# Performance work log

Measured on AMD Instinct MI355X. Metric: run time of the kernel, lower is better.

## Reference

```python
import jax, jax.numpy as jnp
import numpy as np

DIM = 512
NUM_HEADS = 16
HEAD_DIM = DIM // NUM_HEADS
WINDOW = 256
MEM = 16  # memory tokens
NEG_INF = -1e30


def setup_inputs() -> dict:
    key = jax.random.key(0)
    ks = jax.random.split(key, 12)
    B, S, D = 2, 2048, DIM
    inp = {
        "query": jax.random.normal(ks[0], (B, S, D), jnp.float32),
        "key": jax.random.normal(ks[1], (B, S, D), jnp.float32),
        "value": jax.random.normal(ks[2], (B, S, D), jnp.float32),
        # persistent memory tokens, init N(0, 0.02)
        "mem": 0.02 * jax.random.normal(ks[3], (1, MEM, D), jnp.float32),
        # linear layers (stored as [in, out]; x @ W + b)
        "Wq": jax.random.normal(ks[4], (D, D), jnp.float32) / np.sqrt(D),
        "bq": jnp.zeros((D,), jnp.float32),
        "Wk": jax.random.normal(ks[5], (D, D), jnp.float32) / np.sqrt(D),
        "bk": jnp.zeros((D,), jnp.float32),
        "Wv": jax.random.normal(ks[6], (D, D), jnp.float32) / np.sqrt(D),
        "bv": jnp.zeros((D,), jnp.float32),
        "Wo": jax.random.normal(ks[7], (D, D), jnp.float32) / np.sqrt(D),
        "bo": jnp.zeros((D,), jnp.float32),
    }
    return inp


def _sliding_mask(seq_len):
    # additive mask for [MEM + seq_len] tokens: memory rows/cols fully visible,
    # content-content limited to |i-j| <= window//2
    T = seq_len + MEM
    w2 = WINDOW // 2
    i = jnp.arange(T)[:, None]
    j = jnp.arange(T)[None, :]
    allowed = (i < MEM) | (j < MEM) | (jnp.abs(i - j) <= w2)
    return jnp.where(allowed, 0.0, NEG_INF).astype(jnp.float32)


def reference(query, key, value, mem, Wq, bq, Wk, bk, Wv, bv, Wo, bo):
    B, S, D = query.shape
    scale = HEAD_DIM ** -0.5
    m = jnp.broadcast_to(mem, (B, MEM, D))
    qm = jnp.concatenate([m, query], axis=1)  # [B, T, D]
    km = jnp.concatenate([m, key], axis=1)
    vm = jnp.concatenate([m, value], axis=1)
    T = S + MEM

    def heads(x, W, b):
        y = x @ W + b
        return y.reshape(B, T, NUM_HEADS, HEAD_DIM).transpose(0, 2, 1, 3)  # [B,H,T,hd]

    q = heads(qm, Wq, bq)
    k = heads(km, Wk, bk)
    v = heads(vm, Wv, bv)

    mask = _sliding_mask(S)[None, None]  # [1,1,T,T]
    scores = jnp.einsum("bhqd,bhkd->bhqk", q, k) * scale + mask
    weights = jax.nn.softmax(scores, axis=-1)
    ctx = jnp.einsum("bhqk,bhkd->bhqd", weights, v)
    ctx = ctx.transpose(0, 2, 1, 3).reshape(B, T, D)
    ctx = ctx[:, MEM:]  # drop memory tokens
    return ctx @ Wo + bo
```

## Files before the change

### kernel.cpp

```cpp
#include <hip/hip_runtime.h>
#include <hip/hip_bf16.h>
#include <hip/hip_fp16.h>

#define DIM 512
#define NUM_HEADS 16
#define HEAD_DIM 32
#define WHALF 128
#define MEMN 16
#define SEQ 2048
#define BATCH 2
#define T_TOT (SEQ + MEMN)
#define MROWS (BATCH * T_TOT)
#define OROWS (BATCH * SEQ)
#define QT 128
#define MAXU 416
#define KSTR 40
#define VSTR 424

typedef _Float16 f16x8 __attribute__((ext_vector_type(8)));
typedef __fp16   f16raw2 __attribute__((ext_vector_type(2)));
typedef float    f32x4 __attribute__((ext_vector_type(4)));

#define QSCALE 0.17677669529663687f

__global__ __launch_bounds__(256) void prep_cvt(
    const float* __restrict__ q, const float* __restrict__ k,
    const float* __restrict__ v, const float* __restrict__ memp,
    const float* __restrict__ Wq, const float* __restrict__ Wk,
    const float* __restrict__ Wv, const float* __restrict__ Wo,
    ushort* __restrict__ Xq, ushort* __restrict__ Xk, ushort* __restrict__ Xv,
    ushort* __restrict__ Wtq, ushort* __restrict__ Wtk,
    ushort* __restrict__ Wtv, ushort* __restrict__ Wto)
{
    const int z = blockIdx.z;
    if (z < 3) {
        const float* X = z == 0 ? q : (z == 1 ? k : v);
        ushort*     Xc = z == 0 ? Xq : (z == 1 ? Xk : Xv);
        const int gid  = blockIdx.x * 256 + threadIdx.x;
        const int base = gid * 8;
        if (base >= MROWS * DIM) return;
        const int row = base >> 9;
        const int c   = base & 511;
        const int b   = row / T_TOT;
        const int t   = row - b * T_TOT;
        const float* src = (t < MEMN)
            ? (memp + (size_t)t * DIM + c)
            : (X + ((size_t)b * SEQ + (t - MEMN)) * DIM + c);
        const float4 a0 = *(const float4*)src;
        const float4 a1 = *(const float4*)(src + 4);
        union { _Float16 hh[8]; uint4 u4; } o;
        o.hh[0] = (_Float16)a0.x; o.hh[1] = (_Float16)a0.y;
        o.hh[2] = (_Float16)a0.z; o.hh[3] = (_Float16)a0.w;
        o.hh[4] = (_Float16)a1.x; o.hh[5] = (_Float16)a1.y;
        o.hh[6] = (_Float16)a1.z; o.hh[7] = (_Float16)a1.w;
        *(uint4*)(Xc + (size_t)row * DIM + c) = o.u4;
        return;
    }
    if (blockIdx.x >= 64) return;
    const int w = z - 3;
    const float* W  = w == 0 ? Wq  : (w == 1 ? Wk  : (w == 2 ? Wv  : Wo));
    ushort*     Wt  = w == 0 ? Wtq : (w == 1 ? Wtk : (w == 2 ? Wtv : Wto));
    const float ws  = (w == 0) ? QSCALE : 1.0f;

    __shared__ float sT[64][65];
    const int n0 = (blockIdx.x & 7) * 64;
    const int k0 = (blockIdx.x >> 3) * 64;

    for (int e = threadIdx.x; e < 1024; e += 256) {
        const int r  = e >> 4;
        const int c4 = e & 15;
        const float4 f = *(const float4*)(W + (size_t)(k0 + r) * DIM + n0 + c4 * 4);
        sT[r][c4 * 4 + 0] = f.x;
        sT[r][c4 * 4 + 1] = f.y;
        sT[r][c4 * 4 + 2] = f.z;
        sT[r][c4 * 4 + 3] = f.w;
    }
    __syncthreads();
    for (int u = threadIdx.x; u < 512; u += 256) {
        const int n  = u >> 3;
        const int kg = u & 7;
        union { ushort us[8]; uint4 u4; } o;
        #pragma unroll
        for (int j = 0; j < 8; ++j) {
            _Float16 h = (_Float16)(sT[kg * 8 + j][n] * ws);
            o.us[j] = *(ushort*)&h;
        }
        *(uint4*)(Wt + (size_t)(n0 + n) * DIM + k0 + kg * 8) = o.u4;
    }
}

__device__ __forceinline__ void gemm_body128(
    const ushort* __restrict__ A, const ushort* __restrict__ Bt,
    const float* __restrict__ bias, float bscale, ushort* __restrict__ C, int M)
{
    __shared__ _Float16 sA[128][72];
    __shared__ _Float16 sB[128][72];

    const int tid  = threadIdx.x;
    const int row0 = blockIdx.x * 128;
    const int col0 = blockIdx.y * 128;
    const int wave = tid >> 6, lane = tid & 63;
    const int wr = wave >> 1, wc = wave & 1;
    const int fr = lane & 15, fq = lane >> 4;

    f32x4 acc[4][4];
    #pragma unroll
    for (int n = 0; n < 4; ++n) {
        const float bb = bias[col0 + wc * 64 + n * 16 + fr] * bscale;
        #pragma unroll
        for (int m = 0; m < 4; ++m) acc[m][n] = (f32x4){bb, bb, bb, bb};
    }

    for (int k0 = 0; k0 < 512; k0 += 64) {
        __syncthreads();
        #pragma unroll
        for (int it = 0; it < 8; ++it) {
            const int u  = tid + it * 256;
            const int r  = (u >> 3) & 127;
            const int cc = u & 7;
            if (u < 1024) {
                int gr = row0 + r; if (gr >= M) gr = M - 1;
                *(uint4*)&sA[r][cc * 8] =
                    *(const uint4*)(A + (size_t)gr * 512 + k0 + cc * 8);
            } else {
                *(uint4*)&sB[r][cc * 8] =
                    *(const uint4*)(Bt + (size_t)(col0 + r) * 512 + k0 + cc * 8);
            }
        }
        __syncthreads();
        #pragma unroll
        for (int kk = 0; kk < 2; ++kk) {
            f16x8 a[4], b[4];
            #pragma unroll
            for (int m = 0; m < 4; ++m)
                a[m] = *(const f16x8*)&sA[wr * 64 + m * 16 + fr][kk * 32 + fq * 8];
            #pragma unroll
            for (int n = 0; n < 4; ++n)
                b[n] = *(const f16x8*)&sB[wc * 64 + n * 16 + fr][kk * 32 + fq * 8];
            #pragma unroll
            for (int m = 0; m < 4; ++m)
                #pragma unroll
                for (int n = 0; n < 4; ++n)
                    acc[m][n] = __builtin_amdgcn_mfma_f32_16x16x32_f16(
                        a[m], b[n], acc[m][n], 0, 0, 0);
        }
    }

    #pragma unroll
    for (int m = 0; m < 4; ++m)
        #pragma unroll
        for (int n = 0; n < 4; ++n)
            #pragma unroll
            for (int j = 0; j < 4; ++j) {
                const int row = row0 + wr * 64 + m * 16 + fq * 4 + j;
                const int col = col0 + wc * 64 + n * 16 + fr;
                if (row < M) {
                    _Float16 h = (_Float16)acc[m][n][j];
                    C[(size_t)row * 512 + col] = *(ushort*)&h;
                }
            }
}

__global__ __launch_bounds__(256) void gemm_qkv(
    const ushort* __restrict__ Xq, const ushort* __restrict__ Xk,
    const ushort* __restrict__ Xv,
    const ushort* __restrict__ Wtq, const ushort* __restrict__ Wtk,
    const ushort* __restrict__ Wtv,
    const float* __restrict__ bq, const float* __restrict__ bk,
    const float* __restrict__ bv,
    ushort* __restrict__ Qc, ushort* __restrict__ Kc, ushort* __restrict__ Vc)
{
    const int w = blockIdx.z;
    const ushort* A  = w == 0 ? Xq  : (w == 1 ? Xk  : Xv);
    const ushort* Bt = w == 0 ? Wtq : (w == 1 ? Wtk : Wtv);
    const float*  bi = w == 0 ? bq  : (w == 1 ? bk  : bv);
    ushort*       Cc = w == 0 ? Qc  : (w == 1 ? Kc  : Vc);
    gemm_body128(A, Bt, bi, (w == 0) ? QSCALE : 1.0f, Cc, MROWS);
}

__global__ __launch_bounds__(256) void gemm_out64(
    const ushort* __restrict__ A, const ushort* __restrict__ Bt,
    const float* __restrict__ bias, float* __restrict__ C)
{
    __shared__ _Float16 sA[64][72];
    __shared__ _Float16 sB[128][72];

    const int tid  = threadIdx.x;
    const int row0 = blockIdx.x * 64;
    const int col0 = blockIdx.y * 128;
    const int wave = tid >> 6, lane = tid & 63;
    const int wr = wave >> 1, wc = wave & 1;
    const int fr = lane & 15, fq = lane >> 4;

    f32x4 acc[2][4];
    #pragma unroll
    for (int n = 0; n < 4; ++n) {
        const float bb = bias[col0 + wc * 64 + n * 16 + fr];
        #pragma unroll
        for (int m = 0; m < 2; ++m) acc[m][n] = (f32x4){bb, bb, bb, bb};
    }

    for (int k0 = 0; k0 < 512; k0 += 64) {
        __syncthreads();
        #pragma unroll
        for (int it = 0; it < 6; ++it) {
            const int u  = tid + it * 256;
            const int cc = u & 7;
            if (u < 512) {
                const int r = u >> 3;
                *(uint4*)&sA[r][cc * 8] =
                    *(const uint4*)(A + (size_t)(row0 + r) * 512 + k0 + cc * 8);
            } else {
                const int r = (u - 512) >> 3;
                *(uint4*)&sB[r][cc * 8] =
                    *(const uint4*)(Bt + (size_t)(col0 + r) * 512 + k0 + cc * 8);
            }
        }
        __syncthreads();
        #pragma unroll
        for (int kk = 0; kk < 2; ++kk) {
            f16x8 a[2], b[4];
            #pragma unroll
            for (int m = 0; m < 2; ++m)
                a[m] = *(const f16x8*)&sA[wr * 32 + m * 16 + fr][kk * 32 + fq * 8];
            #pragma unroll
            for (int n = 0; n < 4; ++n)
                b[n] = *(const f16x8*)&sB[wc * 64 + n * 16 + fr][kk * 32 + fq * 8];
            #pragma unroll
            for (int m = 0; m < 2; ++m)
                #pragma unroll
                for (int n = 0; n < 4; ++n)
                    acc[m][n] = __builtin_amdgcn_mfma_f32_16x16x32_f16(
                        a[m], b[n], acc[m][n], 0, 0, 0);
        }
    }

    #pragma unroll
    for (int m = 0; m < 2; ++m)
        #pragma unroll
        for (int n = 0; n < 4; ++n)
            #pragma unroll
            for (int j = 0; j < 4; ++j) {
                const int row = row0 + wr * 32 + m * 16 + fq * 4 + j;
                const int col = col0 + wc * 64 + n * 16 + fr;
                C[(size_t)row * 512 + col] = acc[m][n][j];
            }
}

__global__ __launch_bounds__(512, 4) void attn_mfma(
    const ushort* __restrict__ Q, const ushort* __restrict__ K,
    const ushort* __restrict__ V, ushort* __restrict__ ctx)
{
    const int tid  = threadIdx.x;
    const int tile = blockIdx.x, h = blockIdx.y, b = blockIdx.z;
    const int wave = tid >> 6, lane = tid & 63;
    const int fr = lane & 15, fq = lane >> 4;
    const int fq8 = fq * 8, fq4 = fq * 4;

    const int i0  = MEMN + tile * QT;
    const int klo = max(MEMN, i0 - WHALF);
    const int khi = min(T_TOT - 1, i0 + QT - 1 + WHALF);
    const int total  = MEMN + khi - klo + 1;
    const int ustage = (total + 31) & ~31;

    __shared__ ushort sK[MAXU][KSTR];
    __shared__ ushort sVt[HEAD_DIM][VSTR];

    const size_t hbase = (size_t)b * T_TOT * DIM + (size_t)h * HEAD_DIM;

    for (int idx = tid; idx < ustage * 4; idx += 512) {
        const int u = idx >> 2, c = idx & 3;
        const int cc = (c + u) & 3;
        uint4 val = {0, 0, 0, 0};
        if (u < total) {
            const int g = (u < MEMN) ? u : klo + u - MEMN;
            val = *(const uint4*)(K + hbase + (size_t)g * DIM + cc * 8);
        }
        *(uint4*)&sK[u][cc * 8] = val;
    }
    for (int idx = tid; idx < (ustage / 2) * 4; idx += 512) {
        const int pr = idx >> 2;
        const int u2 = pr * 2, c = idx & 3;
        union { uint4 q4; ushort us[8]; } r0, r1;
        r0.q4 = (uint4){0, 0, 0, 0};
        r1.q4 = (uint4){0, 0, 0, 0};
        if (u2 < total) {
            const int g0 = (u2 < MEMN) ? u2 : klo + u2 - MEMN;
            r0.q4 = *(const uint4*)(V + hbase + (size_t)g0 * DIM + c * 8);
        }
        if (u2 + 1 < total) {
            const int g1 = (u2 + 1 < MEMN) ? u2 + 1 : klo + u2 + 1 - MEMN;
            r1.q4 = *(const uint4*)(V + hbase + (size_t)g1 * DIM + c * 8);
        }
        const int g  = u2 & 31, gb = u2 & ~31;
        const int w  = (g < 16) ? ((g >> 2) * 4 + ((g >> 1) & 1))
                                : (((g - 16) >> 2) * 4 + 2 + (((g - 16) >> 1) & 1));
        const int col = gb + w * 2;
        #pragma unroll
        for (int ii = 0; ii < 8; ++ii) {
            const int i = (ii + pr + 2 * c) & 7;
            const uint wv = (uint)r0.us[i] | ((uint)r1.us[i] << 16);
            *(uint*)&sVt[c * 8 + i][col] = wv;
        }
    }

    const int iq = i0 + wave * 16 + fr;
    const f16x8 qf = *(const f16x8*)(Q + (size_t)(b * T_TOT + iq) * DIM
                                     + h * HEAD_DIM + fq8);

    const int ulo  = max(iq - WHALF - klo, 0) + MEMN;
    const int uhi  = min(iq + WHALF, khi) - klo + MEMN;
    const int span = uhi - ulo;
    const int iw0  = i0 + wave * 16;
    const int ulo_minw = max(iw0 - WHALF - klo, 0) + MEMN;
    const int ulo_maxw = max(iw0 + 15 - WHALF - klo, 0) + MEMN;
    const int uhi_minw = min(iw0 + WHALF, khi) - klo + MEMN;
    const int uhi_maxw = min(iw0 + 15 + WHALF, khi) - klo + MEMN;
    const int glo = max(1, ulo_minw >> 5);
    const int ghi = uhi_maxw >> 5;

    __syncthreads();

    const float NEGINF = -__builtin_huge_valf();
    float mns = 0.0f;
    float l   = 0.f;
    f32x4 oc0 = {0, 0, 0, 0}, oc1 = {0, 0, 0, 0};

    {
        const f16x8 kfA = *(const f16x8*)&sK[fr][fq8];
        const f16x8 kfB = *(const f16x8*)&sK[16 + fr][fq8];
        f32x4 sA = {0, 0, 0, 0}, sB = {0, 0, 0, 0};
        sA = __builtin_amdgcn_mfma_f32_16x16x32_f16(kfA, qf, sA, 0, 0, 0);
        sB = __builtin_amdgcn_mfma_f32_16x16x32_f16(kfB, qf, sB, 0, 0, 0);
        if (!(16 >= ulo_maxw && 31 <= uhi_minw)) {
            #pragma unroll
            for (int j = 0; j < 4; ++j) {
                const uint uu = (uint)(16 + fq4 + j - ulo);
                sB[j] = (uu <= (uint)span) ? sB[j] : NEGINF;
            }
        }
        float mx = fmaxf(fmaxf(fmaxf(sA[0], sA[1]), fmaxf(sA[2], sA[3])),
                         fmaxf(fmaxf(sB[0], sB[1]), fmaxf(sB[2], sB[3])));
        mx = fmaxf(mx, __shfl_xor(mx, 16));
        mx = fmaxf(mx, __shfl_xor(mx, 32));
        if (!__all(mx <= mns)) {
            const float mn2   = fmaxf(mns, mx);
            const float alpha = __expf(mns - mn2);
            l *= alpha;
            #pragma unroll
            for (int j = 0; j < 4; ++j) { oc0[j] *= alpha; oc1[j] *= alpha; }
            mns = mn2;
        }
        const float p0 = __expf(sA[0] - mns), p1 = __expf(sA[1] - mns);
        const float p2 = __expf(sA[2] - mns), p3 = __expf(sA[3] - mns);
        const float p4 = __expf(sB[0] - mns), p5 = __expf(sB[1] - mns);
        const float p6 = __expf(sB[2] - mns), p7 = __expf(sB[3] - mns);
        l += ((p0 + p1) + (p2 + p3)) + ((p4 + p5) + (p6 + p7));
        union { f16raw2 h2; uint u; } c0, c1, c2, c3;
        c0.h2 = __builtin_amdgcn_cvt_pkrtz(p0, p1);
        c1.h2 = __builtin_amdgcn_cvt_pkrtz(p2, p3);
        c2.h2 = __builtin_amdgcn_cvt_pkrtz(p4, p5);
        c3.h2 = __builtin_amdgcn_cvt_pkrtz(p6, p7);
        union { uint u[4]; f16x8 h; } P;
        P.u[0] = c0.u; P.u[1] = c1.u; P.u[2] = c2.u; P.u[3] = c3.u;
        const f16x8 va0 = *(const f16x8*)&sVt[fr][fq8];
        const f16x8 va1 = *(const f16x8*)&sVt[fr + 16][fq8];
        oc0 = __builtin_amdgcn_mfma_f32_16x16x32_f16(va0, P.h, oc0, 0, 0, 0);
        oc1 = __builtin_amdgcn_mfma_f32_16x16x32_f16(va1, P.h, oc1, 0, 0, 0);
    }

    int g = glo;
    for (; g + 1 <= ghi; g += 2) {
        const int ua = g * 32, ub2 = ua + 32;
        const f16x8 kf0 = *(const f16x8*)&sK[ua + fr][fq8];
        const f16x8 kf1 = *(const f16x8*)&sK[ua + 16 + fr][fq8];
        const f16x8 kf2 = *(const f16x8*)&sK[ub2 + fr][fq8];
        const f16x8 kf3 = *(const f16x8*)&sK[ub2 + 16 + fr][fq8];
        f32x4 s0 = {0,0,0,0}, s1 = {0,0,0,0}, s2 = {0,0,0,0}, s3 = {0,0,0,0};
        s0 = __builtin_amdgcn_mfma_f32_16x16x32_f16(kf0, qf, s0, 0, 0, 0);
        s1 = __builtin_amdgcn_mfma_f32_16x16x32_f16(kf1, qf, s1, 0, 0, 0);
        s2 = __builtin_amdgcn_mfma_f32_16x16x32_f16(kf2, qf, s2, 0, 0, 0);
        s3 = __builtin_amdgcn_mfma_f32_16x16x32_f16(kf3, qf, s3, 0, 0, 0);
        #pragma unroll
        for (int cch = 0; cch < 4; ++cch) {
            const int base = ua + cch * 16;
            f32x4& sc = cch == 0 ? s0 : (cch == 1 ? s1 : (cch == 2 ? s2 : s3));
            if (!(base >= ulo_maxw && base + 15 <= uhi_minw)) {
                #pragma unroll
                for (int j = 0; j < 4; ++j) {
                    const uint uu = (uint)(base + fq4 + j - ulo);
                    sc[j] = (uu <= (uint)span) ? sc[j] : NEGINF;
                }
            }
        }
        float mxA = fmaxf(fmaxf(fmaxf(s0[0], s0[1]), fmaxf(s0[2], s0[3])),
                          fmaxf(fmaxf(s1[0], s1[1]), fmaxf(s1[2], s1[3])));
        float mxB = fmaxf(fmaxf(fmaxf(s2[0], s2[1]), fmaxf(s2[2], s2[3])),
                          fmaxf(fmaxf(s3[0], s3[1]), fmaxf(s3[2], s3[3])));
        float mx = fmaxf(mxA, mxB);
        mx = fmaxf(mx, __shfl_xor(mx, 16));
        mx = fmaxf(mx, __shfl_xor(mx, 32));
        if (!__all(mx <= mns)) {
            const float mn2   = fmaxf(mns, mx);
            const float alpha = __expf(mns - mn2);
            l *= alpha;
            #pragma unroll
            for (int j = 0; j < 4; ++j) { oc0[j] *= alpha; oc1[j] *= alpha; }
            mns = mn2;
        }
        const float a0 = __expf(s0[0] - mns), a1 = __expf(s0[1] - mns);
        const float a2 = __expf(s0[2] - mns), a3 = __expf(s0[3] - mns);
        const float a4 = __expf(s1[0] - mns), a5 = __expf(s1[1] - mns);
        const float a6 = __expf(s1[2] - mns), a7 = __expf(s1[3] - mns);
        const float b0 = __expf(s2[0] - mns), b1 = __expf(s2[1] - mns);
        const float b2 = __expf(s2[2] - mns), b3 = __expf(s2[3] - mns);
        const float b4 = __expf(s3[0] - mns), b5 = __expf(s3[1] - mns);
        const float b6 = __expf(s3[2] - mns), b7 = __expf(s3[3] - mns);
        l += (((a0 + a1) + (a2 + a3)) + ((a4 + a5) + (a6 + a7)))
           + (((b0 + b1) + (b2 + b3)) + ((b4 + b5) + (b6 + b7)));
        union { f16raw2 h2; uint u; } d0, d1, d2, d3, e0, e1, e2, e3;
        d0.h2 = __builtin_amdgcn_cvt_pkrtz(a0, a1);
        d1.h2 = __builtin_amdgcn_cvt_pkrtz(a2, a3);
        d2.h2 = __builtin_amdgcn_cvt_pkrtz(a4, a5);
        d3.h2 = __builtin_amdgcn_cvt_pkrtz(a6, a7);
        e0.h2 = __builtin_amdgcn_cvt_pkrtz(b0, b1);
        e1.h2 = __builtin_amdgcn_cvt_pkrtz(b2, b3);
        e2.h2 = __builtin_amdgcn_cvt_pkrtz(b4, b5);
        e3.h2 = __builtin_amdgcn_cvt_pkrtz(b6, b7);
        union { uint u[4]; f16x8 h; } P0, P1;
        P0.u[0] = d0.u; P0.u[1] = d1.u; P0.u[2] = d2.u; P0.u[3] = d3.u;
        P1.u[0] = e0.u; P1.u[1] = e1.u; P1.u[2] = e2.u; P1.u[3] = e3.u;
        const f16x8 va0a = *(const f16x8*)&sVt[fr][ua + fq8];
        const f16x8 va1a = *(const f16x8*)&sVt[fr + 16][ua + fq8];
        const f16x8 va0b = *(const f16x8*)&sVt[fr][ub2 + fq8];
        const f16x8 va1b = *(const f16x8*)&sVt[fr + 16][ub2 + fq8];
        oc0 = __builtin_amdgcn_mfma_f32_16x16x32_f16(va0a, P0.h, oc0, 0, 0, 0);
        oc1 = __builtin_amdgcn_mfma_f32_16x16x32_f16(va1a, P0.h, oc1, 0, 0, 0);
        oc0 = __builtin_amdgcn_mfma_f32_16x16x32_f16(va0b, P1.h, oc0, 0, 0, 0);
        oc1 = __builtin_amdgcn_mfma_f32_16x16x32_f16(va1b, P1.h, oc1, 0, 0, 0);
    }
    if (g <= ghi) {
        const int ua = g * 32;
        const f16x8 kf0 = *(const f16x8*)&sK[ua + fr][fq8];
        const f16x8 kf1 = *(const f16x8*)&sK[ua + 16 + fr][fq8];
        f32x4 s0 = {0,0,0,0}, s1 = {0,0,0,0};
        s0 = __builtin_amdgcn_mfma_f32_16x16x32_f16(kf0, qf, s0, 0, 0, 0);
        s1 = __builtin_amdgcn_mfma_f32_16x16x32_f16(kf1, qf, s1, 0, 0, 0);
        #pragma unroll
        for (int cch = 0; cch < 2; ++cch) {
            const int base = ua + cch * 16;
            f32x4& sc = cch == 0 ? s0 : s1;
            if (!(base >= ulo_maxw && base + 15 <= uhi_minw)) {
                #pragma unroll
                for (int j = 0; j < 4; ++j) {
                    const uint uu = (uint)(base + fq4 + j - ulo);
                    sc[j] = (uu <= (uint)span) ? sc[j] : NEGINF;
                }
            }
        }
        float mx = fmaxf(fmaxf(fmaxf(s0[0], s0[1]), fmaxf(s0[2], s0[3])),
                         fmaxf(fmaxf(s1[0], s1[1]), fmaxf(s1[2], s1[3])));
        mx = fmaxf(mx, __shfl_xor(mx, 16));
        mx = fmaxf(mx, __shfl_xor(mx, 32));
        if (!__all(mx <= mns)) {
            const float mn2   = fmaxf(mns, mx);
            const float alpha = __expf(mns - mn2);
            l *= alpha;
            #pragma unroll
            for (int j = 0; j < 4; ++j) { oc0[j] *= alpha; oc1[j] *= alpha; }
            mns = mn2;
        }
        const float p0 = __expf(s0[0] - mns), p1 = __expf(s0[1] - mns);
        const float p2 = __expf(s0[2] - mns), p3 = __expf(s0[3] - mns);
        const float p4 = __expf(s1[0] - mns), p5 = __expf(s1[1] - mns);
        const float p6 = __expf(s1[2] - mns), p7 = __expf(s1[3] - mns);
        l += ((p0 + p1) + (p2 + p3)) + ((p4 + p5) + (p6 + p7));
        union { f16raw2 h2; uint u; } c0, c1, c2, c3;
        c0.h2 = __builtin_amdgcn_cvt_pkrtz(p0, p1);
        c1.h2 = __builtin_amdgcn_cvt_pkrtz(p2, p3);
        c2.h2 = __builtin_amdgcn_cvt_pkrtz(p4, p5);
        c3.h2 = __builtin_amdgcn_cvt_pkrtz(p6, p7);
        union { uint u[4]; f16x8 h; } P;
        P.u[0] = c0.u; P.u[1] = c1.u; P.u[2] = c2.u; P.u[3] = c3.u;
        const f16x8 va0 = *(const f16x8*)&sVt[fr][ua + fq8];
        const f16x8 va1 = *(const f16x8*)&sVt[fr + 16][ua + fq8];
        oc0 = __builtin_amdgcn_mfma_f32_16x16x32_f16(va0, P.h, oc0, 0, 0, 0);
        oc1 = __builtin_amdgcn_mfma_f32_16x16x32_f16(va1, P.h, oc1, 0, 0, 0);
    }

    l += __shfl_xor(l, 16);
    l += __shfl_xor(l, 32);
    const float inv = 1.0f / l;
    union { f16raw2 h2; uint u; } w00, w01, w10, w11;
    w00.h2 = __builtin_amdgcn_cvt_pkrtz(oc0[0] * inv, oc0[1] * inv);
    w01.h2 = __builtin_amdgcn_cvt_pkrtz(oc0[2] * inv, oc0[3] * inv);
    w10.h2 = __builtin_amdgcn_cvt_pkrtz(oc1[0] * inv, oc1[1] * inv);
    w11.h2 = __builtin_amdgcn_cvt_pkrtz(oc1[2] * inv, oc1[3] * inv);
    ushort* cp = ctx + ((size_t)b * SEQ + (iq - MEMN)) * DIM
               + h * HEAD_DIM + fq4;
    *(uint2*)cp        = (uint2){w00.u, w01.u};
    *(uint2*)(cp + 16) = (uint2){w10.u, w11.u};
}

extern "C" void kernel_launch(void* const* d_in, const int* in_sizes, int n_in,
                              void* d_out, int out_size, void* d_ws, size_t ws_size,
                              hipStream_t stream) {
    const float* q    = (const float*)d_in[0];
    const float* k    = (const float*)d_in[1];
    const float* v    = (const float*)d_in[2];
    const float* memp = (const float*)d_in[3];
    const float* Wq   = (const float*)d_in[4];
    const float* bq   = (const float*)d_in[5];
    const float* Wk   = (const float*)d_in[6];
    const float* bk   = (const float*)d_in[7];
    const float* Wv   = (const float*)d_in[8];
    const float* bv   = (const float*)d_in[9];
    const float* Wo   = (const float*)d_in[10];
    const float* bo   = (const float*)d_in[11];
    float* out = (float*)d_out;

    const size_t NX = (size_t)MROWS * DIM;
    const size_t NW = (size_t)DIM * DIM;
    const size_t NC = (size_t)OROWS * DIM;

    ushort* p   = (ushort*)d_ws;
    ushort* Xq  = p;            p += NX;
    ushort* Xk  = p;            p += NX;
    ushort* Xv  = p;            p += NX;
    ushort* Qc  = p;            p += NX;
    ushort* Kc  = p;            p += NX;
    ushort* Vc  = p;            p += NX;
    ushort* Wtq = p;            p += NW;
    ushort* Wtk = p;            p += NW;
    ushort* Wtv = p;            p += NW;
    ushort* Wto = p;            p += NW;
    ushort* Cc  = p;            p += NC;

    dim3 gp((MROWS * DIM / 8 + 255) / 256, 1, 7);
    prep_cvt<<<gp, 256, 0, stream>>>(q, k, v, memp, Wq, Wk, Wv, Wo,
                                     Xq, Xk, Xv, Wtq, Wtk, Wtv, Wto);

    dim3 g1((MROWS + 127) / 128, 4, 3);
    gemm_qkv<<<g1, 256, 0, stream>>>(Xq, Xk, Xv, Wtq, Wtk, Wtv,
                                     bq, bk, bv, Qc, Kc, Vc);

    dim3 g2(SEQ / QT, NUM_HEADS, BATCH);
    attn_mfma<<<g2, 512, 0, stream>>>(Qc, Kc, Vc, Cc);

    dim3 g3(OROWS / 64, 4, 1);
    gemm_out64<<<g3, 256, 0, stream>>>(Cc, Wto, bo, out);
}
```

Before: 80.68 us.

## Store V row-major and read transposed via ds_read_b64_tr_b16; shrink QKV GEMM tiles

The attention kernel now stages V row-major in two 16-column planes and uses the gfx950 LDS transpose-read instruction to build the MFMA A-operand. This replaces the scalar transposing scatter into sVt during staging. The transposed reads are issued early, with an explicit lgkmcnt wait placed before the PV MFMAs. Separately, the QKV GEMM switches to 64-row tiles through a shared templated body that the output GEMM also uses, which doubles the grid for better CU occupancy at the cost of more reloading of B tiles.

```diff
diff --git a/kernel.cpp b/kernel.cpp
--- a/kernel.cpp
+++ b/kernel.cpp
@@ -15,13 +15,20 @@
 #define QT 128
 #define MAXU 416
 #define KSTR 40
-#define VSTR 424
+#define VPLANE (MAXU * 16 * 2)
 
 typedef _Float16 f16x8 __attribute__((ext_vector_type(8)));
 typedef __fp16   f16raw2 __attribute__((ext_vector_type(2)));
 typedef float    f32x4 __attribute__((ext_vector_type(4)));
+typedef uint     u32x2 __attribute__((ext_vector_type(2)));
 
 #define QSCALE 0.17677669529663687f
+
+__device__ __forceinline__ u32x2 tr64(uint addr) {
+    u32x2 r;
+    asm volatile("ds_read_b64_tr_b16 %0, %1" : "=v"(r) : "v"(addr));
+    return r;
+}
 
 __global__ __launch_bounds__(256) void prep_cvt(
     const float* __restrict__ q, const float* __restrict__ k,
@@ -89,40 +96,42 @@
     }
 }
 
-__device__ __forceinline__ void gemm_body128(
+template<bool OUT_HALF>
+__device__ __forceinline__ void gemm_body64(
     const ushort* __restrict__ A, const ushort* __restrict__ Bt,
-    const float* __restrict__ bias, float bscale, ushort* __restrict__ C, int M)
+    const float* __restrict__ bias, float bscale, void* __restrict__ C, int M)
 {
-    __shared__ _Float16 sA[128][72];
+    __shared__ _Float16 sA[64][72];
     __shared__ _Float16 sB[128][72];
 
     const int tid  = threadIdx.x;
-    const int row0 = blockIdx.x * 128;
+    const int row0 = blockIdx.x * 64;
     const int col0 = blockIdx.y * 128;
     const int wave = tid >> 6, lane = tid & 63;
     const int wr = wave >> 1, wc = wave & 1;
     const int fr = lane & 15, fq = lane >> 4;
 
-    f32x4 acc[4][4];
+    f32x4 acc[2][4];
     #pragma unroll
     for (int n = 0; n < 4; ++n) {
         const float bb = bias[col0 + wc * 64 + n * 16 + fr] * bscale;
         #pragma unroll
-        for (int m = 0; m < 4; ++m) acc[m][n] = (f32x4){bb, bb, bb, bb};
+        for (int m = 0; m < 2; ++m) acc[m][n] = (f32x4){bb, bb, bb, bb};
     }
 
     for (int k0 = 0; k0 < 512; k0 += 64) {
         __syncthreads();
         #pragma unroll
-        for (int it = 0; it < 8; ++it) {
+        for (int it = 0; it < 6; ++it) {
             const int u  = tid + it * 256;
-            const int r  = (u >> 3) & 127;
             const int cc = u & 7;
-            if (u < 1024) {
+            if (u < 512) {
+                const int r = u >> 3;
                 int gr = row0 + r; if (gr >= M) gr = M - 1;
                 *(uint4*)&sA[r][cc * 8] =
                     *(const uint4*)(A + (size_t)gr * 512 + k0 + cc * 8);
             } else {
+                const int r = (u - 512) >> 3;
                 *(uint4*)&sB[r][cc * 8] =
                     *(const uint4*)(Bt + (size_t)(col0 + r) * 512 + k0 + cc * 8);
             }
@@ -130,15 +139,15 @@
         __syncthreads();
         #pragma unroll
         for (int kk = 0; kk < 2; ++kk) {
-            f16x8 a[4], b[4];
-            #pragma unroll
-            for (int m = 0; m < 4; ++m)
-                a[m] = *(const f16x8*)&sA[wr * 64 + m * 16 + fr][kk * 32 + fq * 8];
+            f16x8 a[2], b[4];
+            #pragma unroll
+            for (int m = 0; m < 2; ++m)
+                a[m] = *(const f16x8*)&sA[wr * 32 + m * 16 + fr][kk * 32 + fq * 8];
             #pragma unroll
             for (int n = 0; n < 4; ++n)
                 b[n] = *(const f16x8*)&sB[wc * 64 + n * 16 + fr][kk * 32 + fq * 8];
             #pragma unroll
-            for (int m = 0; m < 4; ++m)
+            for (int m = 0; m < 2; ++m)
                 #pragma unroll
                 for (int n = 0; n < 4; ++n)
                     acc[m][n] = __builtin_amdgcn_mfma_f32_16x16x32_f16(
@@ -147,16 +156,20 @@
     }
 
     #pragma unroll
-    for (int m = 0; m < 4; ++m)
+    for (int m = 0; m < 2; ++m)
         #pragma unroll
         for (int n = 0; n < 4; ++n)
             #pragma unroll
             for (int j = 0; j < 4; ++j) {
-                const int row = row0 + wr * 64 + m * 16 + fq * 4 + j;
+                const int row = row0 + wr * 32 + m * 16 + fq * 4 + j;
                 const int col = col0 + wc * 64 + n * 16 + fr;
                 if (row < M) {
-                    _Float16 h = (_Float16)acc[m][n][j];
-                    C[(size_t)row * 512 + col] = *(ushort*)&h;
+                    if (OUT_HALF) {
+                        _Float16 h = (_Float16)acc[m][n][j];
+                        ((ushort*)C)[(size_t)row * 512 + col] = *(ushort*)&h;
+                    } else {
+                        ((float*)C)[(size_t)row * 512 + col] = acc[m][n][j];
+                    }
                 }
             }
 }
@@ -175,76 +188,14 @@
     const ushort* Bt = w == 0 ? Wtq : (w == 1 ? Wtk : Wtv);
     const float*  bi = w == 0 ? bq  : (w == 1 ? bk  : bv);
     ushort*       Cc = w == 0 ? Qc  : (w == 1 ? Kc  : Vc);
-    gemm_body128(A, Bt, bi, (w == 0) ? QSCALE : 1.0f, Cc, MROWS);
+    gemm_body64<true>(A, Bt, bi, (w == 0) ? QSCALE : 1.0f, Cc, MROWS);
 }
 
 __global__ __launch_bounds__(256) void gemm_out64(
     const ushort* __restrict__ A, const ushort* __restrict__ Bt,
     const float* __restrict__ bias, float* __restrict__ C)
 {
-    __shared__ _Float16 sA[64][72];
-    __shared__ _Float16 sB[128][72];
-
-    const int tid  = threadIdx.x;
-    const int row0 = blockIdx.x * 64;
-    const int col0 = blockIdx.y * 128;
-    const int wave = tid >> 6, lane = tid & 63;
-    const int wr = wave >> 1, wc = wave & 1;
-    const int fr = lane & 15, fq = lane >> 4;
-
-    f32x4 acc[2][4];
-    #pragma unroll
-    for (int n = 0; n < 4; ++n) {
-        const float bb = bias[col0 + wc * 64 + n * 16 + fr];
-        #pragma unroll
-        for (int m = 0; m < 2; ++m) acc[m][n] = (f32x4){bb, bb, bb, bb};
-    }
-
-    for (int k0 = 0; k0 < 512; k0 += 64) {
-        __syncthreads();
-        #pragma unroll
-        for (int it = 0; it < 6; ++it) {
-            const int u  = tid + it * 256;
-            const int cc = u & 7;
-            if (u < 512) {
-                const int r = u >> 3;
-                *(uint4*)&sA[r][cc * 8] =
-                    *(const uint4*)(A + (size_t)(row0 + r) * 512 + k0 + cc * 8);
-            } else {
-                const int r = (u - 512) >> 3;
-                *(uint4*)&sB[r][cc * 8] =
-                    *(const uint4*)(Bt + (size_t)(col0 + r) * 512 + k0 + cc * 8);
-            }
-        }
-        __syncthreads();
-        #pragma unroll
-        for (int kk = 0; kk < 2; ++kk) {
-            f16x8 a[2], b[4];
-            #pragma unroll
-            for (int m = 0; m < 2; ++m)
-                a[m] = *(const f16x8*)&sA[wr * 32 + m * 16 + fr][kk * 32 + fq * 8];
-            #pragma unroll
-            for (int n = 0; n < 4; ++n)
-                b[n] = *(const f16x8*)&sB[wc * 64 + n * 16 + fr][kk * 32 + fq * 8];
-            #pragma unroll
-            for (int m = 0; m < 2; ++m)
-                #pragma unroll
-                for (int n = 0; n < 4; ++n)
-                    acc[m][n] = __builtin_amdgcn_mfma_f32_16x16x32_f16(
-                        a[m], b[n], acc[m][n], 0, 0, 0);
-        }
-    }
-
-    #pragma unroll
-    for (int m = 0; m < 2; ++m)
-        #pragma unroll
-        for (int n = 0; n < 4; ++n)
-            #pragma unroll
-            for (int j = 0; j < 4; ++j) {
-                const int row = row0 + wr * 32 + m * 16 + fq * 4 + j;
-                const int col = col0 + wc * 64 + n * 16 + fr;
-                C[(size_t)row * 512 + col] = acc[m][n][j];
-            }
+    gemm_body64<false>(A, Bt, bias, 1.0f, C, OROWS);
 }
 
 __global__ __launch_bounds__(512, 4) void attn_mfma(
@@ -264,44 +215,29 @@
     const int ustage = (total + 31) & ~31;
 
     __shared__ ushort sK[MAXU][KSTR];
-    __shared__ ushort sVt[HEAD_DIM][VSTR];
+    __shared__ ushort sV[2][MAXU][16];
 
     const size_t hbase = (size_t)b * T_TOT * DIM + (size_t)h * HEAD_DIM;
 
     for (int idx = tid; idx < ustage * 4; idx += 512) {
         const int u = idx >> 2, c = idx & 3;
-        const int cc = (c + u) & 3;
         uint4 val = {0, 0, 0, 0};
         if (u < total) {
             const int g = (u < MEMN) ? u : klo + u - MEMN;
-            val = *(const uint4*)(K + hbase + (size_t)g * DIM + cc * 8);
-        }
-        *(uint4*)&sK[u][cc * 8] = val;
-    }
-    for (int idx = tid; idx < (ustage / 2) * 4; idx += 512) {
-        const int pr = idx >> 2;
-        const int u2 = pr * 2, c = idx & 3;
-        union { uint4 q4; ushort us[8]; } r0, r1;
-        r0.q4 = (uint4){0, 0, 0, 0};
-        r1.q4 = (uint4){0, 0, 0, 0};
-        if (u2 < total) {
-            const int g0 = (u2 < MEMN) ? u2 : klo + u2 - MEMN;
-            r0.q4 = *(const uint4*)(V + hbase + (size_t)g0 * DIM + c * 8);
-        }
-        if (u2 + 1 < total) {
-            const int g1 = (u2 + 1 < MEMN) ? u2 + 1 : klo + u2 + 1 - MEMN;
-            r1.q4 = *(const uint4*)(V + hbase + (size_t)g1 * DIM + c * 8);
-        }
-        const int g  = u2 & 31, gb = u2 & ~31;
-        const int w  = (g < 16) ? ((g >> 2) * 4 + ((g >> 1) & 1))
-                                : (((g - 16) >> 2) * 4 + 2 + (((g - 16) >> 1) & 1));
-        const int col = gb + w * 2;
-        #pragma unroll
-        for (int ii = 0; ii < 8; ++ii) {
-            const int i = (ii + pr + 2 * c) & 7;
-            const uint wv = (uint)r0.us[i] | ((uint)r1.us[i] << 16);
-            *(uint*)&sVt[c * 8 + i][col] = wv;
-        }
+            val = *(const uint4*)(K + hbase + (size_t)g * DIM + c * 8);
+        }
+        *(uint4*)&sK[u][c * 8] = val;
+    }
+    for (int idx = tid; idx < ustage * 4; idx += 512) {
+        const int pl   = (idx >= ustage * 2) ? 1 : 0;
+        const int s    = idx - pl * ustage * 2;
+        const int u    = s >> 1, half = s & 1;
+        uint4 val = {0, 0, 0, 0};
+        if (u < total) {
+            const int g = (u < MEMN) ? u : klo + u - MEMN;
+            val = *(const uint4*)(V + hbase + (size_t)g * DIM + pl * 16 + half * 8);
+        }
+        *(uint4*)&sV[pl][u][half * 8] = val;
     }
 
     const int iq = i0 + wave * 16 + fr;
@@ -319,6 +255,8 @@
     const int glo = max(1, ulo_minw >> 5);
     const int ghi = uhi_maxw >> 5;
 
+    const uint vlane = (uint)(size_t)(&sV[0][0][0]) + (uint)(lane * 8);
+
     __syncthreads();
 
     const float NEGINF = -__builtin_huge_valf();
@@ -332,6 +270,9 @@
         f32x4 sA = {0, 0, 0, 0}, sB = {0, 0, 0, 0};
         sA = __builtin_amdgcn_mfma_f32_16x16x32_f16(kfA, qf, sA, 0, 0, 0);
         sB = __builtin_amdgcn_mfma_f32_16x16x32_f16(kfB, qf, sB, 0, 0, 0);
+        const uint vb = vlane;
+        u32x2 t0 = tr64(vb), t1 = tr64(vb + 512);
+        u32x2 t2 = tr64(vb + VPLANE), t3 = tr64(vb + VPLANE + 512);
         if (!(16 >= ulo_maxw && 31 <= uhi_minw)) {
             #pragma unroll
             for (int j = 0; j < 4; ++j) {
@@ -363,10 +304,13 @@
         c3.h2 = __builtin_amdgcn_cvt_pkrtz(p6, p7);
         union { uint u[4]; f16x8 h; } P;
         P.u[0] = c0.u; P.u[1] = c1.u; P.u[2] = c2.u; P.u[3] = c3.u;
-        const f16x8 va0 = *(const f16x8*)&sVt[fr][fq8];
-        const f16x8 va1 = *(const f16x8*)&sVt[fr + 16][fq8];
-        oc0 = __builtin_amdgcn_mfma_f32_16x16x32_f16(va0, P.h, oc0, 0, 0, 0);
-        oc1 = __builtin_amdgcn_mfma_f32_16x16x32_f16(va1, P.h, oc1, 0, 0, 0);
+        asm volatile("s_waitcnt lgkmcnt(0)" ::: "memory");
+        __builtin_amdgcn_sched_barrier(0);
+        union { u32x2 d[2]; f16x8 h; } VA0, VA1;
+        VA0.d[0] = t0; VA0.d[1] = t1;
+        VA1.d[0] = t2; VA1.d[1] = t3;
+        oc0 = __builtin_amdgcn_mfma_f32_16x16x32_f16(VA0.h, P.h, oc0, 0, 0, 0);
+        oc1 = __builtin_amdgcn_mfma_f32_16x16x32_f16(VA1.h, P.h, oc1, 0, 0, 0);
     }
 
     int g = glo;
@@ -381,6 +325,11 @@
         s1 = __builtin_amdgcn_mfma_f32_16x16x32_f16(kf1, qf, s1, 0, 0, 0);
         s2 = __builtin_amdgcn_mfma_f32_16x16x32_f16(kf2, qf, s2, 0, 0, 0);
         s3 = __builtin_amdgcn_mfma_f32_16x16x32_f16(kf3, qf, s3, 0, 0, 0);
+        const uint vb = vlane + (uint)(ua * 32);
+        u32x2 ta0 = tr64(vb),          ta1 = tr64(vb + 512);
+        u32x2 ta2 = tr64(vb + VPLANE), ta3 = tr64(vb + VPLANE + 512);
+        u32x2 tb0 = tr64(vb + 1024),          tb1 = tr64(vb + 1536);
+        u32x2 tb2 = tr64(vb + VPLANE + 1024), tb3 = tr64(vb + VPLANE + 1536);
         #pragma unroll
         for (int cch = 0; cch < 4; ++cch) {
             const int base = ua + cch * 16;
@@ -430,14 +379,17 @@
         union { uint u[4]; f16x8 h; } P0, P1;
         P0.u[0] = d0.u; P0.u[1] = d1.u; P0.u[2] = d2.u; P0.u[3] = d3.u;
         P1.u[0] = e0.u; P1.u[1] = e1.u; P1.u[2] = e2.u; P1.u[3] = e3.u;
-        const f16x8 va0a = *(const f16x8*)&sVt[fr][ua + fq8];
-        const f16x8 va1a = *(const f16x8*)&sVt[fr + 16][ua + fq8];
-        const f16x8 va0b = *(const f16x8*)&sVt[fr][ub2 + fq8];
-        const f16x8 va1b = *(const f16x8*)&sVt[fr + 16][ub2 + fq8];
-        oc0 = __builtin_amdgcn_mfma_f32_16x16x32_f16(va0a, P0.h, oc0, 0, 0, 0);
-        oc1 = __builtin_amdgcn_mfma_f32_16x16x32_f16(va1a, P0.h, oc1, 0, 0, 0);
-        oc0 = __builtin_amdgcn_mfma_f32_16x16x32_f16(va0b, P1.h, oc0, 0, 0, 0);
-        oc1 = __builtin_amdgcn_mfma_f32_16x16x32_f16(va1b, P1.h, oc1, 0, 0, 0);
+        asm volatile("s_waitcnt lgkmcnt(0)" ::: "memory");
+        __builtin_amdgcn_sched_barrier(0);
+        union { u32x2 d[2]; f16x8 h; } A0, A1, B0, B1;
+        A0.d[0] = ta0; A0.d[1] = ta1;
+        A1.d[0] = ta2; A1.d[1] = ta3;
+        B0.d[0] = tb0; B0.d[1] = tb1;
+        B1.d[0] = tb2; B1.d[1] = tb3;
+        oc0 = __builtin_amdgcn_mfma_f32_16x16x32_f16(A0.h, P0.h, oc0, 0, 0, 0);
+        oc1 = __builtin_amdgcn_mfma_f32_16x16x32_f16(A1.h, P0.h, oc1, 0, 0, 0);
+        oc0 = __builtin_amdgcn_mfma_f32_16x16x32_f16(B0.h, P1.h, oc0, 0, 0, 0);
+        oc1 = __builtin_amdgcn_mfma_f32_16x16x32_f16(B1.h, P1.h, oc1, 0, 0, 0);
     }
     if (g <= ghi) {
         const int ua = g * 32;
@@ -446,6 +398,9 @@
         f32x4 s0 = {0,0,0,0}, s1 = {0,0,0,0};
         s0 = __builtin_amdgcn_mfma_f32_16x16x32_f16(kf0, qf, s0, 0, 0, 0);
         s1 = __builtin_amdgcn_mfma_f32_16x16x32_f16(kf1, qf, s1, 0, 0, 0);
+        const uint vb = vlane + (uint)(ua * 32);
+        u32x2 t0 = tr64(vb),          t1 = tr64(vb + 512);
+        u32x2 t2 = tr64(vb + VPLANE), t3 = tr64(vb + VPLANE + 512);
         #pragma unroll
         for (int cch = 0; cch < 2; ++cch) {
             const int base = ua + cch * 16;
@@ -482,10 +437,13 @@
         c3.h2 = __builtin_amdgcn_cvt_pkrtz(p6, p7);
         union { uint u[4]; f16x8 h; } P;
         P.u[0] = c0.u; P.u[1] = c1.u; P.u[2] = c2.u; P.u[3] = c3.u;
-        const f16x8 va0 = *(const f16x8*)&sVt[fr][ua + fq8];
-        const f16x8 va1 = *(const f16x8*)&sVt[fr + 16][ua + fq8];
-        oc0 = __builtin_amdgcn_mfma_f32_16x16x32_f16(va0, P.h, oc0, 0, 0, 0);
-        oc1 = __builtin_amdgcn_mfma_f32_16x16x32_f16(va1, P.h, oc1, 0, 0, 0);
+        asm volatile("s_waitcnt lgkmcnt(0)" ::: "memory");
+        __builtin_amdgcn_sched_barrier(0);
+        union { u32x2 d[2]; f16x8 h; } VA0, VA1;
+        VA0.d[0] = t0; VA0.d[1] = t1;
+        VA1.d[0] = t2; VA1.d[1] = t3;
+        oc0 = __builtin_amdgcn_mfma_f32_16x16x32_f16(VA0.h, P.h, oc0, 0, 0, 0);
+        oc1 = __builtin_amdgcn_mfma_f32_16x16x32_f16(VA1.h, P.h, oc1, 0, 0, 0);
     }
 
     l += __shfl_xor(l, 16);
@@ -540,7 +498,7 @@
     prep_cvt<<<gp, 256, 0, stream>>>(q, k, v, memp, Wq, Wk, Wv, Wo,
                                      Xq, Xk, Xv, Wtq, Wtk, Wtv, Wto);
 
-    dim3 g1((MROWS + 127) / 128, 4, 3);
+    dim3 g1((MROWS + 63) / 64, 4, 3);
     gemm_qkv<<<g1, 256, 0, stream>>>(Xq, Xk, Xv, Wtq, Wtk, Wtv,
                                      bq, bk, bv, Qc, Kc, Vc);
 
```

After: 65.34 us. 19.0% less time.
